# Performance work log

Measured on AMD Instinct MI355X. Metric: run time of the kernel, lower is better.

Reference implementation:

```python
import jax, jax.numpy as jnp
import numpy as np

B, S, D, H = 2, 2048, 1024, 16
DK = D // H


def setup_inputs() -> dict:
    key = jax.random.key(0)
    ks = jax.random.split(key, 12)
    scale = 1.0 / np.sqrt(D)
    inp = {
        "query": jax.random.normal(ks[0], (B, S, D), jnp.float32),
        "key_in": jax.random.normal(ks[1], (B, S, D), jnp.float32),
        "value": jax.random.normal(ks[2], (B, S, D), jnp.float32),
        "mask": jnp.ones((1, 1, S, S), dtype=bool),
        "w_q": jax.random.normal(ks[3], (D, D), jnp.float32) * scale,
        "b_q": jnp.zeros((D,), jnp.float32),
        "w_k": jax.random.normal(ks[4], (D, D), jnp.float32) * scale,
        "b_k": jnp.zeros((D,), jnp.float32),
        "w_v": jax.random.normal(ks[5], (D, D), jnp.float32) * scale,
        "b_v": jnp.zeros((D,), jnp.float32),
        "w_o": jax.random.normal(ks[6], (D, D), jnp.float32) * scale,
        "b_o": jnp.zeros((D,), jnp.float32),
    }
    return inp


def reference(query, key_in, value, mask, w_q, b_q, w_k, b_k, w_v, b_v, w_o, b_o):
    # QKV projections (nn.Linear: x @ W.T + b; here weights stored as [D_in, D_out])
    q = query @ w_q + b_q          # [B, S, D]
    k = key_in @ w_k + b_k
    v = value @ w_v + b_v
    # split heads -> [B, H, S, DK]
    q = q.reshape(B, S, H, DK).transpose(0, 2, 1, 3)
    k = k.reshape(B, S, H, DK).transpose(0, 2, 1, 3)
    v = v.reshape(B, S, H, DK).transpose(0, 2, 1, 3)
    # scaled dot-product attention (naive: full [B,H,S,S] scores)
    scores = jnp.einsum('bhqd,bhkd->bhqk', q, k) / jnp.sqrt(jnp.float32(DK))
    scores = jnp.where(mask, scores, jnp.float32(-1e9))
    probs = jax.nn.softmax(scores, axis=-1)  # dropout p=0.0 -> identity
    x = jnp.einsum('bhqk,bhkd->bhqd', probs, v)  # [B, H, S, DK]
    x = x.transpose(0, 2, 1, 3).reshape(B, S, D)
    return x @ w_o + b_o
```

## Files before the change

kernel.cpp:

```cpp
#include <hip/hip_runtime.h>
#include <cstdint>
#include <cstddef>


typedef _Float16 f16_t;
typedef _Float16 f16x8 __attribute__((ext_vector_type(8)));
typedef _Float16 f16x4 __attribute__((ext_vector_type(4)));
typedef float    f32x4 __attribute__((ext_vector_type(4)));
typedef unsigned int u32x2 __attribute__((ext_vector_type(2)));

#define S_LEN 2048
#define DMODEL 1024
#define NHEAD 16
#define DK 64
#define NKV (S_LEN / 64)

__device__ __forceinline__ void async_copy16(void* lds, const void* g) {
    __builtin_amdgcn_global_load_lds(
        (const __attribute__((address_space(1))) unsigned int*)g,
        (__attribute__((address_space(3))) unsigned int*)lds,
        16, 0, 0);
}

__device__ __forceinline__ float fexp2(float x) {
#if __has_builtin(__builtin_amdgcn_exp2f)
    return __builtin_amdgcn_exp2f(x);
#else
    return exp2f(x);
#endif
}

__device__ __forceinline__ unsigned int cvt_pk_u32(float a, float b) {
#if __has_builtin(__builtin_amdgcn_cvt_pkrtz)
    return __builtin_bit_cast(unsigned int, __builtin_amdgcn_cvt_pkrtz(a, b));
#else
    union { f16_t h[2]; unsigned int u; } r;
    r.h[0] = (f16_t)a; r.h[1] = (f16_t)b; return r.u;
#endif
}

__global__ __launch_bounds__(256) void prep_kernel(
    const float* __restrict__ q_in, const float* __restrict__ k_in, const float* __restrict__ v_in,
    f16_t* __restrict__ xq, f16_t* __restrict__ xk, f16_t* __restrict__ xv, int n,
    const float* __restrict__ w0, const float* __restrict__ w1,
    const float* __restrict__ w2, const float* __restrict__ w3,
    f16_t* __restrict__ wt_base)
{
    __shared__ float tile[32][33];
    int bid = blockIdx.x;
    if (bid < 12288) {
        int z  = bid >> 12;
        int bx = bid & 4095;
        const float* s = z == 0 ? q_in : z == 1 ? k_in : v_in;
        f16_t*       d = z == 0 ? xq   : z == 1 ? xk   : xv;
        int i = (bx * 256 + threadIdx.x) * 4;
        if (i + 3 < n) {
            f32x4 v = *(const f32x4*)(s + i);
            f16x4 o;
            o[0] = (f16_t)v[0]; o[1] = (f16_t)v[1];
            o[2] = (f16_t)v[2]; o[3] = (f16_t)v[3];
            *(f16x4*)(d + i) = o;
        }
    } else {
        int t  = bid - 12288;
        int z  = t >> 10;
        int tb = t & 1023;
        const float* w = z == 0 ? w0 : z == 1 ? w1 : z == 2 ? w2 : w3;
        f16_t* wt = wt_base + (size_t)z * DMODEL * DMODEL;
        int tx = threadIdx.x & 31, ty = threadIdx.x >> 5;
        int bx = (tb & 31) * 32;
        int by = (tb >> 5) * 32;
#pragma unroll
        for (int i = 0; i < 4; ++i)
            tile[ty + i * 8][tx] = w[(size_t)(bx + ty + i * 8) * DMODEL + by + tx];
        __syncthreads();
#pragma unroll
        for (int i = 0; i < 4; ++i)
            wt[(size_t)(by + ty + i * 8) * DMODEL + bx + tx] = (f16_t)tile[tx][ty + i * 8];
    }
}

__global__ __launch_bounds__(256) void qkv_gemm_kernel(
    const f16_t* __restrict__ Aq, const f16_t* __restrict__ Ak, const f16_t* __restrict__ Av,
    const f16_t* __restrict__ Bt,
    const float* __restrict__ bq, const float* __restrict__ bk, const float* __restrict__ bv,
    f16_t* __restrict__ q_h, f16_t* __restrict__ k_h, f16_t* __restrict__ v_t)
{
    __shared__ f16_t As[128 * 32];
    __shared__ f16_t Bs[128 * 32];

    int tid  = threadIdx.x;
    int lane = tid & 63;
    int w    = tid >> 6;
    int wm   = w >> 1, wn = w & 1;

    int lin = blockIdx.y * 24 + blockIdx.x;
    int swz = (lin & 7) * 96 + (lin >> 3);
    int bx  = swz % 24, by = swz / 24;
    int row0 = by * 128;
    int col0 = bx * 128;
    int which = col0 >> 10;
    const f16_t* A = which == 0 ? Aq : which == 1 ? Ak : Av;
    const float* bias = which == 0 ? bq : which == 1 ? bk : bv;

    f32x4 acc[4][4] = {};

    for (int kk = 0; kk < 1024; kk += 32) {
        __syncthreads();
#pragma unroll
        for (int j = 0; j < 2; ++j) {
            int c = w * 2 + j;
            int r = c * 16 + (lane >> 2);
            int e = (lane & 3) * 8;
            async_copy16(&As[c * 512], A  + (size_t)(row0 + r) * 1024 + kk + e);
            async_copy16(&Bs[c * 512], Bt + (size_t)(col0 + r) * 1024 + kk + e);
        }
        __syncthreads();

        f16x8 a[4], b[4];
#pragma unroll
        for (int mi = 0; mi < 4; ++mi)
            a[mi] = *(const f16x8*)&As[(wm * 64 + mi * 16 + (lane & 15)) * 32 + (lane >> 4) * 8];
#pragma unroll
        for (int ni = 0; ni < 4; ++ni)
            b[ni] = *(const f16x8*)&Bs[(wn * 64 + ni * 16 + (lane & 15)) * 32 + (lane >> 4) * 8];
#pragma unroll
        for (int mi = 0; mi < 4; ++mi)
#pragma unroll
            for (int ni = 0; ni < 4; ++ni)
                acc[mi][ni] = __builtin_amdgcn_mfma_f32_16x16x32_f16(a[mi], b[ni], acc[mi][ni], 0, 0, 0);
    }

    const float QSCALE = 0.125f * 1.4426950408889634f;
#pragma unroll
    for (int mi = 0; mi < 4; ++mi) {
#pragma unroll
        for (int ni = 0; ni < 4; ++ni) {
#pragma unroll
            for (int r = 0; r < 4; ++r) {
                int grow = row0 + wm * 64 + mi * 16 + (lane >> 4) * 4 + r;
                int gcol = col0 + wn * 64 + ni * 16 + (lane & 15);
                int nc   = gcol & 1023;
                float v  = acc[mi][ni][r] + bias[nc];
                int bb = grow >> 11, ss = grow & 2047;
                int hh = nc >> 6,    dd = nc & 63;
                if (which == 0)
                    q_h[(((size_t)(bb * NHEAD + hh) * S_LEN + ss) << 6) + dd] = (f16_t)(v * QSCALE);
                else if (which == 1)
                    k_h[(((size_t)(bb * NHEAD + hh) * S_LEN + ss) << 6) + dd] = (f16_t)v;
                else
                    v_t[((size_t)(bb * NHEAD + hh) * DK + dd) * S_LEN + ss] = (f16_t)v;
            }
        }
    }
}

__global__ __launch_bounds__(512) void out_gemm_kernel(
    const f16_t* __restrict__ A, const f16_t* __restrict__ Bt,
    const float* __restrict__ bias, float* __restrict__ outp)
{
    __shared__ f16_t As[128 * 32];
    __shared__ f16_t Bs[128 * 32];

    int tid  = threadIdx.x;
    int lane = tid & 63;
    int li   = lane & 15;
    int g    = lane >> 4;
    int w    = tid >> 6;
    int wm   = w >> 2, wn = w & 3;

    int lin = blockIdx.y * 8 + blockIdx.x;
    int swz = (lin & 7) * 32 + (lin >> 3);
    int row0 = (swz / 8) * 128;
    int col0 = (swz % 8) * 128;

    f32x4 acc[4][2] = {};

    for (int kk = 0; kk < 1024; kk += 32) {
        __syncthreads();
        {
            int r = w * 16 + (lane >> 2);
            int e = (lane & 3) * 8;
            async_copy16(&As[w * 512], A  + (size_t)(row0 + r) * 1024 + kk + e);
            async_copy16(&Bs[w * 512], Bt + (size_t)(col0 + r) * 1024 + kk + e);
        }
        __syncthreads();

        f16x8 a[4], b[2];
#pragma unroll
        for (int mi = 0; mi < 4; ++mi)
            a[mi] = *(const f16x8*)&As[(wm * 64 + mi * 16 + li) * 32 + g * 8];
#pragma unroll
        for (int ni = 0; ni < 2; ++ni)
            b[ni] = *(const f16x8*)&Bs[(wn * 32 + ni * 16 + li) * 32 + g * 8];
#pragma unroll
        for (int mi = 0; mi < 4; ++mi)
#pragma unroll
            for (int ni = 0; ni < 2; ++ni)
                acc[mi][ni] = __builtin_amdgcn_mfma_f32_16x16x32_f16(a[mi], b[ni], acc[mi][ni], 0, 0, 0);
    }

#pragma unroll
    for (int mi = 0; mi < 4; ++mi)
#pragma unroll
        for (int ni = 0; ni < 2; ++ni)
#pragma unroll
            for (int r = 0; r < 4; ++r) {
                int grow = row0 + wm * 64 + mi * 16 + g * 4 + r;
                int gcol = col0 + wn * 32 + ni * 16 + li;
                outp[(size_t)grow * 1024 + gcol] = acc[mi][ni][r] + bias[gcol];
            }
}

#define PSTR 76

__global__ __launch_bounds__(256) void flash_kernel(
    const f16_t* __restrict__ Q, const f16_t* __restrict__ K,
    const f16_t* __restrict__ Vt, f16_t* __restrict__ Ao)
{
    __shared__ f16_t Kl[2][64 * 64];
    __shared__ f16_t Vl[64 * 64];
    __shared__ f16_t Pw[4][16 * PSTR];

    int tid  = threadIdx.x;
    int lane = tid & 63;
    int li   = lane & 15;
    int g    = lane >> 4;
    int w    = tid >> 6;

    int lin = blockIdx.y * 32 + blockIdx.x;
    int swz = (lin & 7) * 128 + (lin >> 3);
    int qt  = swz & 31;
    int bh  = swz >> 5;

    const size_t hbase = (size_t)bh * S_LEN * DK;
    const f16_t* Qh = Q  + hbase;
    const f16_t* Kh = K  + hbase;
    const f16_t* Vh = Vt + hbase;

    int q0 = qt * 64 + w * 16;

    f16x8 aq[2];
#pragma unroll
    for (int kc = 0; kc < 2; ++kc)
        aq[kc] = *(const f16x8*)(Qh + (size_t)(q0 + li) * DK + kc * 32 + g * 8);

    f16x8 ones;
#pragma unroll
    for (int i = 0; i < 8; ++i) ones[i] = (f16_t)1.0f;

    f32x4 ot[4] = {};
    f32x4 lacc = {};
    float mrun = -1e30f;

    int lr  = lane >> 3;
    int sl8 = ((lane & 7) ^ lr) * 8;
    const f16_t* srcK = Kh + (size_t)(w * 16 + lr) * 64    + sl8;
    const f16_t* srcV = Vh + (size_t)(w * 16 + lr) * S_LEN + sl8;

    auto stageV = [&](int kt) {
        async_copy16(&Vl[(w * 16) * 64],     srcV + kt * 64);
        async_copy16(&Vl[(w * 16 + 8) * 64], srcV + 8 * S_LEN + kt * 64);
    };
    auto stageK = [&](int buf, int kt) {
        const f16_t* p = srcK + (size_t)kt * 4096;
        async_copy16(&Kl[buf][(w * 16) * 64],     p);
        async_copy16(&Kl[buf][(w * 16 + 8) * 64], p + 512);
    };

    int x0 = li * 64 + ((g    ) ^ (li & 7)) * 8;
    int x1 = li * 64 + ((4 + g) ^ (li & 7)) * 8;
    int pww = li * PSTR + g * 4;
    int pwr = li * PSTR + g * 8;

    stageK(0, 0);
    int cur = 0;

    for (int kt = 0; kt < NKV; ++kt) {
        __syncthreads();
        stageV(kt);
        if (kt + 1 < NKV) stageK(cur ^ 1, kt + 1);

        f32x4 s[4] = {};
        __builtin_amdgcn_s_setprio(1);
#pragma unroll
        for (int kc = 0; kc < 2; ++kc)
#pragma unroll
            for (int kn = 0; kn < 4; ++kn) {
                f16x8 ak = *(const f16x8*)&Kl[cur][kn * 1024 + (kc ? x1 : x0)];
                s[kn] = __builtin_amdgcn_mfma_f32_16x16x32_f16(ak, aq[kc], s[kn], 0, 0, 0);
            }
        __builtin_amdgcn_s_setprio(0);

        {
            float mx = fmaxf(s[0][0], s[0][1]);
            mx = fmaxf(fmaxf(mx, s[0][2]), s[0][3]);
            mx = fmaxf(fmaxf(mx, s[1][0]), s[1][1]);
            mx = fmaxf(fmaxf(mx, s[1][2]), s[1][3]);
            mx = fmaxf(fmaxf(mx, s[2][0]), s[2][1]);
            mx = fmaxf(fmaxf(mx, s[2][2]), s[2][3]);
            mx = fmaxf(fmaxf(mx, s[3][0]), s[3][1]);
            mx = fmaxf(fmaxf(mx, s[3][2]), s[3][3]);
            mx = fmaxf(mx, __shfl_xor(mx, 16));
            mx = fmaxf(mx, __shfl_xor(mx, 32));
            if (!__all(mx - mrun <= 8.0f)) {
                float mn = fmaxf(mrun, mx);
                float alpha = fexp2(mrun - mn);
                mrun = mn;
#pragma unroll
                for (int r = 0; r < 4; ++r) lacc[r] *= alpha;
#pragma unroll
                for (int nd = 0; nd < 4; ++nd)
#pragma unroll
                    for (int r = 0; r < 4; ++r)
                        ot[nd][r] *= alpha;
            }
#pragma unroll
            for (int kn = 0; kn < 4; ++kn) {
                u32x2 pv;
                pv[0] = cvt_pk_u32(fexp2(s[kn][0] - mrun), fexp2(s[kn][1] - mrun));
                pv[1] = cvt_pk_u32(fexp2(s[kn][2] - mrun), fexp2(s[kn][3] - mrun));
                *(u32x2*)&Pw[w][pww + kn * 16] = pv;
            }
        }

        if (kt + 1 < NKV) asm volatile("s_waitcnt vmcnt(2)" ::: "memory");
        else              asm volatile("s_waitcnt vmcnt(0)" ::: "memory");

        __builtin_amdgcn_s_setprio(1);
#pragma unroll
        for (int kc = 0; kc < 2; ++kc) {
            f16x8 bp = *(const f16x8*)&Pw[w][pwr + kc * 32];
            lacc = __builtin_amdgcn_mfma_f32_16x16x32_f16(ones, bp, lacc, 0, 0, 0);
#pragma unroll
            for (int nd = 0; nd < 4; ++nd) {
                f16x8 av = *(const f16x8*)&Vl[nd * 1024 + (kc ? x1 : x0)];
                ot[nd] = __builtin_amdgcn_mfma_f32_16x16x32_f16(av, bp, ot[nd], 0, 0, 0);
            }
        }
        __builtin_amdgcn_s_setprio(0);

        cur ^= 1;
    }

    int b = bh >> 4, h = bh & 15;
    {
        float inv = 1.0f / lacc[0];
        int qrow = q0 + li;
        size_t base = (size_t)(b * S_LEN + qrow) * DMODEL + h * 64;
#pragma unroll
        for (int nd = 0; nd < 4; ++nd) {
            f16x4 ov;
#pragma unroll
            for (int r = 0; r < 4; ++r)
                ov[r] = (f16_t)(ot[nd][r] * inv);
            *(f16x4*)&Ao[base + nd * 16 + g * 4] = ov;
        }
    }
}

extern "C" void kernel_launch(void* const* d_in, const int* in_sizes, int n_in,
                              void* d_out, int out_size, void* d_ws, size_t ws_size,
                              hipStream_t stream)
{
    const float* query  = (const float*)d_in[0];
    const float* key_in = (const float*)d_in[1];
    const float* value  = (const float*)d_in[2];
    const float* w_q = (const float*)d_in[4];
    const float* b_q = (const float*)d_in[5];
    const float* w_k = (const float*)d_in[6];
    const float* b_k = (const float*)d_in[7];
    const float* w_v = (const float*)d_in[8];
    const float* b_v = (const float*)d_in[9];
    const float* w_o = (const float*)d_in[10];
    const float* b_o = (const float*)d_in[11];
    float* out = (float*)d_out;

    char* ws = (char*)d_ws;
    const size_t MB = 1024 * 1024;
    f16_t* x_q  = (f16_t*)(ws + 0 * MB);
    f16_t* x_k  = (f16_t*)(ws + 8 * MB);
    f16_t* x_v  = (f16_t*)(ws + 16 * MB);
    f16_t* wt   = (f16_t*)(ws + 24 * MB);
    f16_t* wt_o = (f16_t*)(ws + 30 * MB);
    f16_t* q_h  = (f16_t*)(ws + 32 * MB);
    f16_t* k_h  = (f16_t*)(ws + 40 * MB);
    f16_t* v_t  = (f16_t*)(ws + 48 * MB);
    f16_t* attn = (f16_t*)(ws + 56 * MB);

    const int n = 2 * S_LEN * DMODEL;

    prep_kernel<<<16384, 256, 0, stream>>>(
        query, key_in, value, x_q, x_k, x_v, n, w_q, w_k, w_v, w_o, wt);

    qkv_gemm_kernel<<<dim3(24, 32), 256, 0, stream>>>(
        x_q, x_k, x_v, wt, b_q, b_k, b_v, q_h, k_h, v_t);

    flash_kernel<<<dim3(32, 32), 256, 0, stream>>>(q_h, k_h, v_t, attn);

    out_gemm_kernel<<<dim3(8, 32), 512, 0, stream>>>(attn, wt_o, b_o, out);
}
```

Baseline: 144.0 us.

## Process two 16-row query chunks per warp in flash attention to reuse K/V tiles

Each warp now handles 32 query rows (two 16-row chunks) instead of 16, so each block covers 128 queries. Every K and V fragment loaded from LDS feeds two MFMAs, and the K/V global-to-LDS traffic per query is halved. The grid shrinks from 1024 to 512 blocks. In exchange, register pressure per thread roughly doubles for accumulators and fewer blocks run, which can lower occupancy and latency hiding on a 256-CU device.

New measurement: 140.4 us. 2.5% less time.

```diff
diff --git a/kernel.cpp b/kernel.cpp
--- a/kernel.cpp
+++ b/kernel.cpp
@@ -220,7 +220,7 @@
 {
     __shared__ f16_t Kl[2][64 * 64];
     __shared__ f16_t Vl[64 * 64];
-    __shared__ f16_t Pw[4][16 * PSTR];
+    __shared__ f16_t Pw[4][32 * PSTR];
 
     int tid  = threadIdx.x;
     int lane = tid & 63;
@@ -228,30 +228,32 @@
     int g    = lane >> 4;
     int w    = tid >> 6;
 
-    int lin = blockIdx.y * 32 + blockIdx.x;
-    int swz = (lin & 7) * 128 + (lin >> 3);
-    int qt  = swz & 31;
-    int bh  = swz >> 5;
+    int lin = blockIdx.y * 16 + blockIdx.x;
+    int swz = (lin & 7) * 64 + (lin >> 3);
+    int qt  = swz & 15;
+    int bh  = swz >> 4;
 
     const size_t hbase = (size_t)bh * S_LEN * DK;
     const f16_t* Qh = Q  + hbase;
     const f16_t* Kh = K  + hbase;
     const f16_t* Vh = Vt + hbase;
 
-    int q0 = qt * 64 + w * 16;
-
-    f16x8 aq[2];
-#pragma unroll
-    for (int kc = 0; kc < 2; ++kc)
-        aq[kc] = *(const f16x8*)(Qh + (size_t)(q0 + li) * DK + kc * 32 + g * 8);
+    int q0 = qt * 128 + w * 32;
+
+    f16x8 aq[2][2];
+#pragma unroll
+    for (int qc = 0; qc < 2; ++qc)
+#pragma unroll
+        for (int kc = 0; kc < 2; ++kc)
+            aq[qc][kc] = *(const f16x8*)(Qh + (size_t)(q0 + qc * 16 + li) * DK + kc * 32 + g * 8);
 
     f16x8 ones;
 #pragma unroll
     for (int i = 0; i < 8; ++i) ones[i] = (f16_t)1.0f;
 
-    f32x4 ot[4] = {};
-    f32x4 lacc = {};
-    float mrun = -1e30f;
+    f32x4 ot[2][4] = {};
+    f32x4 lacc[2] = {};
+    float mrun[2] = {-1e30f, -1e30f};
 
     int lr  = lane >> 3;
     int sl8 = ((lane & 7) ^ lr) * 8;
@@ -270,8 +272,6 @@
 
     int x0 = li * 64 + ((g    ) ^ (li & 7)) * 8;
     int x1 = li * 64 + ((4 + g) ^ (li & 7)) * 8;
-    int pww = li * PSTR + g * 4;
-    int pwr = li * PSTR + g * 8;
 
     stageK(0, 0);
     int cur = 0;
@@ -281,45 +281,48 @@
         stageV(kt);
         if (kt + 1 < NKV) stageK(cur ^ 1, kt + 1);
 
-        f32x4 s[4] = {};
+        f32x4 s[4][2] = {};
         __builtin_amdgcn_s_setprio(1);
 #pragma unroll
         for (int kc = 0; kc < 2; ++kc)
 #pragma unroll
             for (int kn = 0; kn < 4; ++kn) {
                 f16x8 ak = *(const f16x8*)&Kl[cur][kn * 1024 + (kc ? x1 : x0)];
-                s[kn] = __builtin_amdgcn_mfma_f32_16x16x32_f16(ak, aq[kc], s[kn], 0, 0, 0);
+                s[kn][0] = __builtin_amdgcn_mfma_f32_16x16x32_f16(ak, aq[0][kc], s[kn][0], 0, 0, 0);
+                s[kn][1] = __builtin_amdgcn_mfma_f32_16x16x32_f16(ak, aq[1][kc], s[kn][1], 0, 0, 0);
             }
         __builtin_amdgcn_s_setprio(0);
 
-        {
-            float mx = fmaxf(s[0][0], s[0][1]);
-            mx = fmaxf(fmaxf(mx, s[0][2]), s[0][3]);
-            mx = fmaxf(fmaxf(mx, s[1][0]), s[1][1]);
-            mx = fmaxf(fmaxf(mx, s[1][2]), s[1][3]);
-            mx = fmaxf(fmaxf(mx, s[2][0]), s[2][1]);
-            mx = fmaxf(fmaxf(mx, s[2][2]), s[2][3]);
-            mx = fmaxf(fmaxf(mx, s[3][0]), s[3][1]);
-            mx = fmaxf(fmaxf(mx, s[3][2]), s[3][3]);
+#pragma unroll
+        for (int qc = 0; qc < 2; ++qc) {
+            float mx = fmaxf(s[0][qc][0], s[0][qc][1]);
+            mx = fmaxf(fmaxf(mx, s[0][qc][2]), s[0][qc][3]);
+            mx = fmaxf(fmaxf(mx, s[1][qc][0]), s[1][qc][1]);
+            mx = fmaxf(fmaxf(mx, s[1][qc][2]), s[1][qc][3]);
+            mx = fmaxf(fmaxf(mx, s[2][qc][0]), s[2][qc][1]);
+            mx = fmaxf(fmaxf(mx, s[2][qc][2]), s[2][qc][3]);
+            mx = fmaxf(fmaxf(mx, s[3][qc][0]), s[3][qc][1]);
+            mx = fmaxf(fmaxf(mx, s[3][qc][2]), s[3][qc][3]);
             mx = fmaxf(mx, __shfl_xor(mx, 16));
             mx = fmaxf(mx, __shfl_xor(mx, 32));
-            if (!__all(mx - mrun <= 8.0f)) {
-                float mn = fmaxf(mrun, mx);
-                float alpha = fexp2(mrun - mn);
-                mrun = mn;
-#pragma unroll
-                for (int r = 0; r < 4; ++r) lacc[r] *= alpha;
+            if (!__all(mx - mrun[qc] <= 8.0f)) {
+                float mn = fmaxf(mrun[qc], mx);
+                float alpha = fexp2(mrun[qc] - mn);
+                mrun[qc] = mn;
+#pragma unroll
+                for (int r = 0; r < 4; ++r) lacc[qc][r] *= alpha;
 #pragma unroll
                 for (int nd = 0; nd < 4; ++nd)
 #pragma unroll
                     for (int r = 0; r < 4; ++r)
-                        ot[nd][r] *= alpha;
-            }
+                        ot[qc][nd][r] *= alpha;
+            }
+            int pww = (qc * 16 + li) * PSTR + g * 4;
 #pragma unroll
             for (int kn = 0; kn < 4; ++kn) {
                 u32x2 pv;
-                pv[0] = cvt_pk_u32(fexp2(s[kn][0] - mrun), fexp2(s[kn][1] - mrun));
-                pv[1] = cvt_pk_u32(fexp2(s[kn][2] - mrun), fexp2(s[kn][3] - mrun));
+                pv[0] = cvt_pk_u32(fexp2(s[kn][qc][0] - mrun[qc]), fexp2(s[kn][qc][1] - mrun[qc]));
+                pv[1] = cvt_pk_u32(fexp2(s[kn][qc][2] - mrun[qc]), fexp2(s[kn][qc][3] - mrun[qc]));
                 *(u32x2*)&Pw[w][pww + kn * 16] = pv;
             }
         }
@@ -330,12 +333,15 @@
         __builtin_amdgcn_s_setprio(1);
 #pragma unroll
         for (int kc = 0; kc < 2; ++kc) {
-            f16x8 bp = *(const f16x8*)&Pw[w][pwr + kc * 32];
-            lacc = __builtin_amdgcn_mfma_f32_16x16x32_f16(ones, bp, lacc, 0, 0, 0);
+            f16x8 bp0 = *(const f16x8*)&Pw[w][(     li) * PSTR + kc * 32 + g * 8];
+            f16x8 bp1 = *(const f16x8*)&Pw[w][(16 + li) * PSTR + kc * 32 + g * 8];
+            lacc[0] = __builtin_amdgcn_mfma_f32_16x16x32_f16(ones, bp0, lacc[0], 0, 0, 0);
+            lacc[1] = __builtin_amdgcn_mfma_f32_16x16x32_f16(ones, bp1, lacc[1], 0, 0, 0);
 #pragma unroll
             for (int nd = 0; nd < 4; ++nd) {
                 f16x8 av = *(const f16x8*)&Vl[nd * 1024 + (kc ? x1 : x0)];
-                ot[nd] = __builtin_amdgcn_mfma_f32_16x16x32_f16(av, bp, ot[nd], 0, 0, 0);
+                ot[0][nd] = __builtin_amdgcn_mfma_f32_16x16x32_f16(av, bp0, ot[0][nd], 0, 0, 0);
+                ot[1][nd] = __builtin_amdgcn_mfma_f32_16x16x32_f16(av, bp1, ot[1][nd], 0, 0, 0);
             }
         }
         __builtin_amdgcn_s_setprio(0);
@@ -344,16 +350,17 @@
     }
 
     int b = bh >> 4, h = bh & 15;
-    {
-        float inv = 1.0f / lacc[0];
-        int qrow = q0 + li;
+#pragma unroll
+    for (int qc = 0; qc < 2; ++qc) {
+        float inv = 1.0f / lacc[qc][0];
+        int qrow = q0 + qc * 16 + li;
         size_t base = (size_t)(b * S_LEN + qrow) * DMODEL + h * 64;
 #pragma unroll
         for (int nd = 0; nd < 4; ++nd) {
             f16x4 ov;
 #pragma unroll
             for (int r = 0; r < 4; ++r)
-                ov[r] = (f16_t)(ot[nd][r] * inv);
+                ov[r] = (f16_t)(ot[qc][nd][r] * inv);
             *(f16x4*)&Ao[base + nd * 16 + g * 4] = ov;
         }
     }
@@ -396,7 +403,7 @@
     qkv_gemm_kernel<<<dim3(24, 32), 256, 0, stream>>>(
         x_q, x_k, x_v, wt, b_q, b_k, b_v, q_h, k_h, v_t);
 
-    flash_kernel<<<dim3(32, 32), 256, 0, stream>>>(q_h, k_h, v_t, attn);
+    flash_kernel<<<dim3(16, 32), 256, 0, stream>>>(q_h, k_h, v_t, attn);
 
     out_gemm_kernel<<<dim3(8, 32), 512, 0, stream>>>(attn, wt_o, b_o, out);
 }
```
